# Kernel optimization log

Measured on AMD Instinct MI355X. Metric: run time of the kernel, lower is better.

## Reference

```python
import jax, jax.numpy as jnp
import numpy as np

N = 100000   # nodes
E = 600000   # edges per graph
F = 512      # node_features == input_size
H = 256      # n_hidden
H2 = 128     # n_hidden // 2
O = 1        # output_size
EPS = 1e-5


def gcn_conv(x, W, b, src, dst, n):
    # PyG GCNConv: add self-loops, symmetric normalization, then scatter-add.
    xw = x @ W                                   # [N, out]
    loop = jnp.arange(n)
    s = jnp.concatenate([src, loop])
    d = jnp.concatenate([dst, loop])
    deg = jax.ops.segment_sum(jnp.ones_like(d, jnp.float32), d, num_segments=n)
    dis = jnp.where(deg > 0, jax.lax.rsqrt(jnp.maximum(deg, 1.0)), 0.0)
    norm = dis[s] * dis[d]                       # [E+N]
    msg = xw[s] * norm[:, None]
    return jax.ops.segment_sum(msg, d, num_segments=n) + b


def sage_conv(x, Wl, bl, Wr, src, dst, n):
    # PyG SAGEConv (mean aggr): lin_l(mean_neigh) + lin_r(x); lin_r has no bias.
    agg = jax.ops.segment_sum(x[src], dst, num_segments=n)
    cnt = jax.ops.segment_sum(jnp.ones_like(dst, jnp.float32), dst, num_segments=n)
    mean = agg / jnp.maximum(cnt, 1.0)[:, None]
    return mean @ Wl + bl + x @ Wr


def layer_norm(x, w, b):
    mu = jnp.mean(x, axis=-1, keepdims=True)
    var = jnp.mean(jnp.square(x - mu), axis=-1, keepdims=True)
    return (x - mu) * jax.lax.rsqrt(var + EPS) * w + b


def mlp(x, Wm1, bm1, ln_w, ln_b, Wm2, bm2):
    h = layer_norm(x @ Wm1 + bm1, ln_w, ln_b)
    return h @ Wm2 + bm2


def setup_inputs() -> dict:
    key = jax.random.key(0)
    ks = jax.random.split(key, 22)
    s = 0.05
    d = {}
    d["x"] = jax.random.normal(ks[0], (N, F), jnp.float32)
    d["x1"] = jax.random.normal(ks[1], (N, F), jnp.float32)
    d["edge_index"] = jax.random.randint(ks[2], (2, E), 0, N)
    d["edge_index1"] = jax.random.randint(ks[3], (2, E), 0, N)
    # conv1_1 / conv2_1: GCNConv(F -> H)
    d["Wg1"] = jax.random.normal(ks[4], (F, H), jnp.float32) * s
    d["bg1"] = jnp.zeros((H,), jnp.float32)
    d["Wg2"] = jax.random.normal(ks[5], (F, H), jnp.float32) * s
    d["bg2"] = jnp.zeros((H,), jnp.float32)
    # conv1_2 / conv2_2: SAGEConv(H -> H2)
    d["Wl1"] = jax.random.normal(ks[6], (H, H2), jnp.float32) * s
    d["bl1"] = jnp.zeros((H2,), jnp.float32)
    d["Wr1"] = jax.random.normal(ks[7], (H, H2), jnp.float32) * s
    d["Wl2"] = jax.random.normal(ks[8], (H, H2), jnp.float32) * s
    d["bl2"] = jnp.zeros((H2,), jnp.float32)
    d["Wr2"] = jax.random.normal(ks[9], (H, H2), jnp.float32) * s
    # shared MLP: Linear(H2,H2) -> LayerNorm(H2) -> Linear(H2,O)
    d["Wm1"] = jax.random.normal(ks[10], (H2, H2), jnp.float32) * s
    d["bm1"] = jnp.zeros((H2,), jnp.float32)
    d["ln_w"] = jnp.ones((H2,), jnp.float32)
    d["ln_b"] = jnp.zeros((H2,), jnp.float32)
    d["Wm2"] = jax.random.normal(ks[11], (H2, O), jnp.float32) * s
    d["bm2"] = jnp.zeros((O,), jnp.float32)
    return d


def reference(x, x1, edge_index, edge_index1, Wg1, bg1, Wg2, bg2,
              Wl1, bl1, Wr1, Wl2, bl2, Wr2, Wm1, bm1, ln_w, ln_b, Wm2, bm2):
    src, dst = edge_index[0], edge_index[1]
    src1, dst1 = edge_index1[0], edge_index1[1]
    n = x.shape[0]

    h = gcn_conv(x, Wg1, bg1, src, dst, n)
    h0 = jax.nn.relu(h)                          # x0 = relu(conv1_1)
    g = gcn_conv(x1, Wg2, bg2, src1, dst1, n)
    g0 = jax.nn.relu(g)                          # x1_0 = relu(conv2_1)

    x0 = h0 + g0
    a = jax.nn.relu(sage_conv(x0, Wl1, bl1, Wr1, src, dst, n))
    a = mlp(a, Wm1, bm1, ln_w, ln_b, Wm2, bm2)   # [N, 1]
    a = jnp.squeeze(a)                            # [N]

    g1 = g0 + g                                   # x1_0 + x1 (pre-relu conv2_1)
    b_ = jax.nn.relu(sage_conv(g1, Wl2, bl2, Wr2, src1, dst1, n))
    b_ = mlp(b_, Wm1, bm1, ln_w, ln_b, Wm2, bm2)
    b_ = jnp.squeeze(b_)                          # [N]

    cat = jnp.concatenate([a, b_], axis=0)        # [2N]
    out = jnp.mean(cat)
    return out[None, None]                        # [1, 1]
```

## Files before the change

kernel.cpp:

```cpp
#include <hip/hip_runtime.h>

#define NN 100000
#define EE 600000
#define FF 512
#define HH 256
#define HD2 128

typedef unsigned short u16;
typedef unsigned int u32;
typedef __attribute__((ext_vector_type(4))) float f32x4;
typedef __attribute__((ext_vector_type(8))) short bf16x8;

__device__ __forceinline__ float bflo(u32 u){ return __uint_as_float(u << 16); }
__device__ __forceinline__ float bfhi(u32 u){ return __uint_as_float(u & 0xffff0000u); }
__device__ __forceinline__ u32 f2bf(float x){
  u32 u = __float_as_uint(x);
  return (u + 0x7FFFu + ((u >> 16) & 1u)) >> 16;
}
__device__ __forceinline__ u32 pack2(float x, float y){ return f2bf(x) | (f2bf(y) << 16); }

__global__ void zero_int_k(int* __restrict__ p, int n){
  int i = blockIdx.x * 256 + threadIdx.x;
  int st = gridDim.x * 256;
  for (; i < n; i += st) p[i] = 0;
}

__global__ void count_deg_k(const int* __restrict__ dst, int* __restrict__ deg, int nE){
  int e = blockIdx.x * 256 + threadIdx.x;
  if (e < nE) atomicAdd(&deg[dst[e]], 1);
}

__global__ __launch_bounds__(256) void scan1_k(const int* __restrict__ deg, int* __restrict__ out,
                                               int* __restrict__ aux, int n){
  __shared__ int sm[256];
  const int t = threadIdx.x;
  const int base = blockIdx.x * 1024 + t * 4;
  int v0 = (base+0) < n ? deg[base+0] : 0;
  int v1 = (base+1) < n ? deg[base+1] : 0;
  int v2 = (base+2) < n ? deg[base+2] : 0;
  int v3 = (base+3) < n ? deg[base+3] : 0;
  int s = v0 + v1 + v2 + v3;
  sm[t] = s;
  __syncthreads();
  for (int off = 1; off < 256; off <<= 1){
    int x = (t >= off) ? sm[t - off] : 0;
    __syncthreads();
    sm[t] += x;
    __syncthreads();
  }
  if (t == 255) aux[blockIdx.x] = sm[255];
  int run = sm[t] - s;
  if (base+0 < n) out[base+0] = run;            run += v0;
  if (base+1 < n) out[base+1] = run;            run += v1;
  if (base+2 < n) out[base+2] = run;            run += v2;
  if (base+3 < n) out[base+3] = run;
}
__global__ void scan2_k(int* __restrict__ aux, int nchunks){
  if (threadIdx.x == 0){
    int run = 0;
    for (int i = 0; i < nchunks; ++i){ int t = aux[i]; aux[i] = run; run += t; }
  }
}
__global__ void scan3_k(int* __restrict__ out, const int* __restrict__ aux, int n){
  int i = blockIdx.x * 256 + threadIdx.x;
  if (i < n) out[i] += aux[i >> 10];
}

__global__ void csr_fill_k(const int* __restrict__ src, const int* __restrict__ dst,
                           const int* __restrict__ rp, int* __restrict__ fill,
                           int* __restrict__ csr, int nE){
  int e = blockIdx.x * 256 + threadIdx.x;
  if (e >= nE) return;
  int d = dst[e];
  int pos = rp[d] + atomicAdd(&fill[d], 1);
  csr[pos] = src[e];
}

__global__ void wtcvt_k(const float* __restrict__ W, u16* __restrict__ WT,
                        int K, int nmask, int nshift, int total){
  int idx = blockIdx.x * 256 + threadIdx.x;
  if (idx >= total) return;
  int k = idx >> nshift, n = idx & nmask;
  WT[(size_t)n * K + k] = (u16)f2bf(W[idx]);
}

__global__ __launch_bounds__(256) void gemm_xw_k(
    const float* __restrict__ A, const u16* __restrict__ BT,
    u16* __restrict__ C, int M)
{
  __shared__ u16 As[128][40];
  __shared__ u16 Bs[128][40];
  const int tid = threadIdx.x;
  const int w = tid >> 6, lane = tid & 63;
  const int row0 = blockIdx.x * 128, col0 = blockIdx.y * 128;
  const int wr = (w >> 1) * 64, wc = (w & 1) * 64;
  const int sar = tid >> 1, sak = (tid & 1) * 16;
  const int lrow = lane & 15, lk = (lane >> 4) * 8;
  f32x4 acc[4][4];
#pragma unroll
  for (int i = 0; i < 4; ++i)
#pragma unroll
    for (int j = 0; j < 4; ++j)
#pragma unroll
      for (int q = 0; q < 4; ++q) acc[i][j][q] = 0.f;

  const bool aval = (row0 + sar) < M;
  const float* apb = A + (size_t)(row0 + sar) * FF + sak;

  for (int kb = 0; kb < FF; kb += 32){
    if (aval){
      const float4* ap = (const float4*)(apb + kb);
      float4 v0 = ap[0], v1 = ap[1], v2 = ap[2], v3 = ap[3];
      uint4 p0 = make_uint4(pack2(v0.x,v0.y), pack2(v0.z,v0.w), pack2(v1.x,v1.y), pack2(v1.z,v1.w));
      uint4 p1 = make_uint4(pack2(v2.x,v2.y), pack2(v2.z,v2.w), pack2(v3.x,v3.y), pack2(v3.z,v3.w));
      *(uint4*)&As[sar][sak]     = p0;
      *(uint4*)&As[sar][sak + 8] = p1;
    } else {
      uint4 z = make_uint4(0,0,0,0);
      *(uint4*)&As[sar][sak]     = z;
      *(uint4*)&As[sar][sak + 8] = z;
    }
    for (int c = tid; c < 512; c += 256){
      int n = c >> 2, part = c & 3;
      uint4 bv = *(const uint4*)(BT + (size_t)(col0 + n) * FF + kb + part * 8);
      *(uint4*)&Bs[n][part * 8] = bv;
    }
    __syncthreads();
    bf16x8 af[4], bfr[4];
#pragma unroll
    for (int mt = 0; mt < 4; ++mt) af[mt]  = *(const bf16x8*)&As[wr + mt*16 + lrow][lk];
#pragma unroll
    for (int nt = 0; nt < 4; ++nt) bfr[nt] = *(const bf16x8*)&Bs[wc + nt*16 + lrow][lk];
#pragma unroll
    for (int mt = 0; mt < 4; ++mt)
#pragma unroll
      for (int nt = 0; nt < 4; ++nt)
        acc[mt][nt] = __builtin_amdgcn_mfma_f32_16x16x32_bf16(af[mt], bfr[nt], acc[mt][nt], 0, 0, 0);
    __syncthreads();
  }
  const int orow = (lane >> 4) * 4, ocol = lane & 15;
#pragma unroll
  for (int mt = 0; mt < 4; ++mt)
#pragma unroll
    for (int i = 0; i < 4; ++i){
      int r = row0 + wr + mt*16 + orow + i;
      if (r < M){
        u16* cp = C + (size_t)r * HH + col0 + wc + ocol;
#pragma unroll
        for (int nt = 0; nt < 4; ++nt)
          cp[nt * 16] = (u16)f2bf(acc[mt][nt][i]);
      }
    }
}

__global__ __launch_bounds__(256) void gcn_agg_k(
    const u16* __restrict__ XW, const int* __restrict__ rp,
    const int* __restrict__ deg, const int* __restrict__ csr,
    const float* __restrict__ bias, u16* __restrict__ H, int n)
{
  const int d = blockIdx.x * 4 + (threadIdx.x >> 6);
  if (d >= n) return;
  const int lane = threadIdx.x & 63;
  const int dg = deg[d];
  const float disd = rsqrtf((float)dg + 1.0f);
  const uint2* xw2 = (const uint2*)XW;
  uint2 sv = xw2[(size_t)d * 64 + lane];
  const float sw = disd * disd;
  float a0 = bflo(sv.x) * sw, a1 = bfhi(sv.x) * sw;
  float a2 = bflo(sv.y) * sw, a3 = bfhi(sv.y) * sw;
  const int s0 = rp[d], s1 = s0 + dg;
  for (int i = s0; i < s1; ++i){
    int s = csr[i];
    float wgt = rsqrtf((float)deg[s] + 1.0f) * disd;
    uint2 v = xw2[(size_t)s * 64 + lane];
    a0 = fmaf(bflo(v.x), wgt, a0); a1 = fmaf(bfhi(v.x), wgt, a1);
    a2 = fmaf(bflo(v.y), wgt, a2); a3 = fmaf(bfhi(v.y), wgt, a3);
  }
  const float4 bv = *(const float4*)(bias + lane * 4);
  a0 += bv.x; a1 += bv.y; a2 += bv.z; a3 += bv.w;
  uint2 o; o.x = pack2(a0, a1); o.y = pack2(a2, a3);
  ((uint2*)H)[(size_t)d * 64 + lane] = o;
}

__global__ __launch_bounds__(256) void sage_mean_k(
    const u16* __restrict__ X, const int* __restrict__ rp,
    const int* __restrict__ deg, const int* __restrict__ csr,
    u16* __restrict__ Mo, int n)
{
  const int d = blockIdx.x * 4 + (threadIdx.x >> 6);
  if (d >= n) return;
  const int lane = threadIdx.x & 63;
  const int dg = deg[d];
  const uint2* x2 = (const uint2*)X;
  float a0 = 0.f, a1 = 0.f, a2 = 0.f, a3 = 0.f;
  const int s0 = rp[d], s1 = s0 + dg;
  for (int i = s0; i < s1; ++i){
    int s = csr[i];
    uint2 v = x2[(size_t)s * 64 + lane];
    a0 += bflo(v.x); a1 += bfhi(v.x);
    a2 += bflo(v.y); a3 += bfhi(v.y);
  }
  const float sc = 1.0f / (float)(dg > 0 ? dg : 1);
  uint2 o; o.x = pack2(a0 * sc, a1 * sc); o.y = pack2(a2 * sc, a3 * sc);
  ((uint2*)Mo)[(size_t)d * 64 + lane] = o;
}

__global__ void combine_k(u32* __restrict__ X0, u32* __restrict__ G1,
                          const u32* __restrict__ H1, const u32* __restrict__ H2)
{
  int i = blockIdx.x * 256 + threadIdx.x;
  u32 uh = H1[i], ug = H2[i];
  float h0 = bflo(uh), h1 = bfhi(uh), g0 = bflo(ug), g1 = bfhi(ug);
  float rh0 = fmaxf(h0, 0.f), rh1 = fmaxf(h1, 0.f);
  float rg0 = fmaxf(g0, 0.f), rg1 = fmaxf(g1, 0.f);
  X0[i] = pack2(rh0 + rg0, rh1 + rg1);
  G1[i] = pack2(rg0 + g0, rg1 + g1);
}

__global__ __launch_bounds__(256) void sage_gemm_k(
    const u16* __restrict__ A1, const u16* __restrict__ A2,
    const u16* __restrict__ B1T, const u16* __restrict__ B2T,
    const float* __restrict__ bias, u16* __restrict__ S, int M)
{
  __shared__ u16 As[128][40];
  __shared__ u16 Bs[128][40];
  const int tid = threadIdx.x;
  const int w = tid >> 6, lane = tid & 63;
  const int row0 = blockIdx.x * 128;
  const int wr = (w >> 1) * 64, wc = (w & 1) * 64;
  const int lrow = lane & 15, lk = (lane >> 4) * 8;
  f32x4 acc[4][4];
#pragma unroll
  for (int i = 0; i < 4; ++i)
#pragma unroll
    for (int j = 0; j < 4; ++j)
#pragma unroll
      for (int q = 0; q < 4; ++q) acc[i][j][q] = 0.f;

  for (int pass = 0; pass < 2; ++pass){
    const u16* Ap = pass ? A2 : A1;
    const u16* Bp = pass ? B2T : B1T;
    for (int kb = 0; kb < HH; kb += 32){
      for (int c = tid; c < 512; c += 256){
        int r = c >> 2, part = c & 3;
        int grow = row0 + r;
        uint4 v = make_uint4(0,0,0,0);
        if (grow < M) v = *(const uint4*)(Ap + (size_t)grow * HH + kb + part * 8);
        *(uint4*)&As[r][part * 8] = v;
      }
      for (int c = tid; c < 512; c += 256){
        int n = c >> 2, part = c & 3;
        uint4 v = *(const uint4*)(Bp + (size_t)n * HH + kb + part * 8);
        *(uint4*)&Bs[n][part * 8] = v;
      }
      __syncthreads();
      bf16x8 af[4], bfr[4];
#pragma unroll
      for (int mt = 0; mt < 4; ++mt) af[mt]  = *(const bf16x8*)&As[wr + mt*16 + lrow][lk];
#pragma unroll
      for (int nt = 0; nt < 4; ++nt) bfr[nt] = *(const bf16x8*)&Bs[wc + nt*16 + lrow][lk];
#pragma unroll
      for (int mt = 0; mt < 4; ++mt)
#pragma unroll
        for (int nt = 0; nt < 4; ++nt)
          acc[mt][nt] = __builtin_amdgcn_mfma_f32_16x16x32_bf16(af[mt], bfr[nt], acc[mt][nt], 0, 0, 0);
      __syncthreads();
    }
  }
  const int orow = (lane >> 4) * 4, ocol = lane & 15;
#pragma unroll
  for (int mt = 0; mt < 4; ++mt)
#pragma unroll
    for (int i = 0; i < 4; ++i){
      int r = row0 + wr + mt*16 + orow + i;
      if (r < M){
        u16* cp = S + (size_t)r * HD2 + wc + ocol;
#pragma unroll
        for (int nt = 0; nt < 4; ++nt){
          float v = acc[mt][nt][i] + bias[wc + nt*16 + ocol];
          cp[nt * 16] = (u16)f2bf(fmaxf(v, 0.f));
        }
      }
    }
}

__global__ __launch_bounds__(256) void mlp_reduce_k(
    const u16* __restrict__ Xin,
    const float* __restrict__ Wm1, const float* __restrict__ bm1,
    const float* __restrict__ lnw, const float* __restrict__ lnb,
    const float* __restrict__ Wm2, const float* __restrict__ bm2,
    double* __restrict__ partial, int M)
{
  __shared__ u32 Wsh[HD2 * HD2 / 2];
  __shared__ float Bsh[HD2];
  __shared__ float LWs[HD2];
  __shared__ float LBs[HD2];
  __shared__ float W2s[HD2];
  __shared__ float arow[4][HD2];
  __shared__ double wsum[4];
  const int tid = threadIdx.x;
  const float2* Wsrc = (const float2*)Wm1;
  for (int i = tid; i < HD2 * HD2 / 2; i += 256){
    float2 w = Wsrc[i];
    Wsh[i] = pack2(w.x, w.y);
  }
  if (tid < HD2){
    Bsh[tid] = bm1[tid];
    LWs[tid] = lnw[tid];
    LBs[tid] = lnb[tid];
    W2s[tid] = Wm2[tid];
  }
  __syncthreads();
  const int lane = tid & 63, wv = tid >> 6;
  const int j0 = lane << 1;
  const float bm2v = bm2[0];
  const u32* xin = (const u32*)Xin;
  double local = 0.0;
  for (int base = blockIdx.x * 4; base < M; base += gridDim.x * 4){
    const int node = base + wv;
    const bool active = node < M;
    if (active){
      u32 u = xin[(size_t)node * 64 + lane];
      arow[wv][j0] = bflo(u);
      arow[wv][j0 + 1] = bfhi(u);
    }
    __syncthreads();
    if (active){
      float2 tb = *(const float2*)&Bsh[j0];
      float t0 = tb.x, t1 = tb.y;
#pragma unroll 8
      for (int k = 0; k < HD2; ++k){
        float ak = arow[wv][k];
        u32 w = Wsh[k * 64 + lane];
        t0 = fmaf(ak, bflo(w), t0);
        t1 = fmaf(ak, bfhi(w), t1);
      }
      float s = t0 + t1;
#pragma unroll
      for (int off = 32; off > 0; off >>= 1) s += __shfl_xor(s, off);
      float mu = s * (1.0f / HD2);
      float v0 = t0 - mu, v1 = t1 - mu;
      float vs = v0 * v0 + v1 * v1;
#pragma unroll
      for (int off = 32; off > 0; off >>= 1) vs += __shfl_xor(vs, off);
      float rs = rsqrtf(vs * (1.0f / HD2) + 1e-5f);
      float2 lw = *(const float2*)&LWs[j0];
      float2 lb = *(const float2*)&LBs[j0];
      float2 w2 = *(const float2*)&W2s[j0];
      float y0 = fmaf(v0 * rs, lw.x, lb.x);
      float y1 = fmaf(v1 * rs, lw.y, lb.y);
      float p = y0 * w2.x + y1 * w2.y;
#pragma unroll
      for (int off = 32; off > 0; off >>= 1) p += __shfl_xor(p, off);
      if (lane == 0) local += (double)(p + bm2v);
    }
    __syncthreads();
  }
  if (lane == 0) wsum[wv] = local;
  __syncthreads();
  if (tid == 0)
    partial[blockIdx.x] = wsum[0] + wsum[1] + wsum[2] + wsum[3];
}

__global__ __launch_bounds__(256) void final_reduce_k(
    const double* __restrict__ P, u32* __restrict__ out)
{
  __shared__ double sm[256];
  const int tid = threadIdx.x;
  double s = P[tid] + P[tid + 256] + P[tid + 512] + P[tid + 768];
  sm[tid] = s;
  __syncthreads();
  for (int h = 128; h > 0; h >>= 1){
    if (tid < h) sm[tid] += sm[tid + h];
    __syncthreads();
  }
  if (tid == 0){
    float v = (float)(sm[0] * (1.0 / (2.0 * (double)NN)));
    u32 bf = f2bf(v);
    out[0] = (bf << 16) | bf;
  }
}

extern "C" void kernel_launch(void* const* d_in, const int* in_sizes, int n_in,
                              void* d_out, int out_size, void* d_ws, size_t ws_size,
                              hipStream_t stream)
{
  const float* x   = (const float*)d_in[0];
  const float* x1  = (const float*)d_in[1];
  const int* ei  = (const int*)d_in[2];
  const int* ei1 = (const int*)d_in[3];
  const float* Wg1 = (const float*)d_in[4];
  const float* bg1 = (const float*)d_in[5];
  const float* Wg2 = (const float*)d_in[6];
  const float* bg2 = (const float*)d_in[7];
  const float* Wl1 = (const float*)d_in[8];
  const float* bl1 = (const float*)d_in[9];
  const float* Wr1 = (const float*)d_in[10];
  const float* Wl2 = (const float*)d_in[11];
  const float* bl2 = (const float*)d_in[12];
  const float* Wr2 = (const float*)d_in[13];
  const float* Wm1 = (const float*)d_in[14];
  const float* bm1 = (const float*)d_in[15];
  const float* lnw = (const float*)d_in[16];
  const float* lnb = (const float*)d_in[17];
  const float* Wm2 = (const float*)d_in[18];
  const float* bm2 = (const float*)d_in[19];

  const int* src1 = ei,  * dst1 = ei + EE;
  const int* src2 = ei1, * dst2 = ei1 + EE;

  u16* U0 = (u16*)d_ws;
  u16* U1 = U0 + (size_t)NN * HH;
  u16* U2 = U1 + (size_t)NN * HH;
  u16* U3 = U2 + (size_t)NN * HH;
  u16* U4 = U3 + (size_t)NN * HH;
  u16* U5 = U4 + (size_t)NN * HD2;
  u16* WG1T = U5 + (size_t)NN * HD2;
  u16* WG2T = WG1T + HH * FF;
  u16* WL1T = WG2T + HH * FF;
  u16* WR1T = WL1T + HD2 * HH;
  u16* WL2T = WR1T + HD2 * HH;
  u16* WR2T = WL2T + HD2 * HH;
  int* deg1 = (int*)(WR2T + HD2 * HH);
  int* deg2 = deg1 + NN;
  int* fill1 = deg2 + NN;
  int* fill2 = fill1 + NN;
  int* rp1 = fill2 + NN;
  int* rp2 = rp1 + NN;
  int* aux1 = rp2 + NN;
  int* aux2 = aux1 + 128;
  int* csr1 = aux2 + 128;
  int* csr2 = csr1 + EE;
  double* P = (double*)(csr2 + EE);

  const int eblk = (EE + 255) / 256;
  const int nchunks = (NN + 1023) / 1024;

  zero_int_k<<<512, 256, 0, stream>>>(deg1, 4 * NN);
  count_deg_k<<<eblk, 256, 0, stream>>>(dst1, deg1, EE);
  count_deg_k<<<eblk, 256, 0, stream>>>(dst2, deg2, EE);
  scan1_k<<<nchunks, 256, 0, stream>>>(deg1, rp1, aux1, NN);
  scan1_k<<<nchunks, 256, 0, stream>>>(deg2, rp2, aux2, NN);
  scan2_k<<<1, 64, 0, stream>>>(aux1, nchunks);
  scan2_k<<<1, 64, 0, stream>>>(aux2, nchunks);
  scan3_k<<<(NN + 255) / 256, 256, 0, stream>>>(rp1, aux1, NN);
  scan3_k<<<(NN + 255) / 256, 256, 0, stream>>>(rp2, aux2, NN);
  csr_fill_k<<<eblk, 256, 0, stream>>>(src1, dst1, rp1, fill1, csr1, EE);
  csr_fill_k<<<eblk, 256, 0, stream>>>(src2, dst2, rp2, fill2, csr2, EE);

  wtcvt_k<<<512, 256, 0, stream>>>(Wg1, WG1T, FF, HH - 1, 8, FF * HH);
  wtcvt_k<<<512, 256, 0, stream>>>(Wg2, WG2T, FF, HH - 1, 8, FF * HH);
  wtcvt_k<<<128, 256, 0, stream>>>(Wl1, WL1T, HH, HD2 - 1, 7, HH * HD2);
  wtcvt_k<<<128, 256, 0, stream>>>(Wr1, WR1T, HH, HD2 - 1, 7, HH * HD2);
  wtcvt_k<<<128, 256, 0, stream>>>(Wl2, WL2T, HH, HD2 - 1, 7, HH * HD2);
  wtcvt_k<<<128, 256, 0, stream>>>(Wr2, WR2T, HH, HD2 - 1, 7, HH * HD2);

  dim3 ggrid((NN + 127) / 128, HH / 128);
  gemm_xw_k<<<ggrid, 256, 0, stream>>>(x,  WG1T, U0, NN);
  gemm_xw_k<<<ggrid, 256, 0, stream>>>(x1, WG2T, U1, NN);

  gcn_agg_k<<<NN / 4, 256, 0, stream>>>(U0, rp1, deg1, csr1, bg1, U2, NN);
  gcn_agg_k<<<NN / 4, 256, 0, stream>>>(U1, rp2, deg2, csr2, bg2, U3, NN);

  combine_k<<<NN * HH / 512, 256, 0, stream>>>((u32*)U0, (u32*)U1, (const u32*)U2, (const u32*)U3);

  sage_mean_k<<<NN / 4, 256, 0, stream>>>(U0, rp1, deg1, csr1, U2, NN);
  sage_mean_k<<<NN / 4, 256, 0, stream>>>(U1, rp2, deg2, csr2, U3, NN);

  sage_gemm_k<<<(NN + 127) / 128, 256, 0, stream>>>(U2, U0, WL1T, WR1T, bl1, U4, NN);
  sage_gemm_k<<<(NN + 127) / 128, 256, 0, stream>>>(U3, U1, WL2T, WR2T, bl2, U5, NN);

  mlp_reduce_k<<<512, 256, 0, stream>>>(U4, Wm1, bm1, lnw, lnb, Wm2, bm2, P, NN);
  mlp_reduce_k<<<512, 256, 0, stream>>>(U5, Wm1, bm1, lnw, lnb, Wm2, bm2, P + 512, NN);

  final_reduce_k<<<1, 256, 0, stream>>>(P, (u32*)d_out);
}
```

Before: 1.531 ms.

## Compute MLP head with bf16 MFMA and fold LayerNorm into final projection

Replaces the scalar per-node MLP kernel with an MFMA-based kernel. Each wave computes 16 nodes at a time against a transposed bf16 Wm1 held in padded shared memory. The LayerNorm affine and the final 128->1 projection are folded algebraically into precomputed constants, so only sums, variance and one dot product are needed per node. Both graph branches are processed in one launch over the contiguous U4/U5 buffers, with U0 reused as scratch for the transposed weight. This trades a small change in rounding order for far fewer LDS reads and scalar FMAs.

```diff
diff --git a/kernel.cpp b/kernel.cpp
--- a/kernel.cpp
+++ b/kernel.cpp
@@ -284,82 +284,95 @@
     }
 }
 
-__global__ __launch_bounds__(256) void mlp_reduce_k(
+__global__ __launch_bounds__(256) void mlp_mfma_k(
     const u16* __restrict__ Xin,
-    const float* __restrict__ Wm1, const float* __restrict__ bm1,
+    const u16* __restrict__ W1T,
+    const float* __restrict__ bm1,
     const float* __restrict__ lnw, const float* __restrict__ lnb,
     const float* __restrict__ Wm2, const float* __restrict__ bm2,
     double* __restrict__ partial, int M)
 {
-  __shared__ u32 Wsh[HD2 * HD2 / 2];
-  __shared__ float Bsh[HD2];
-  __shared__ float LWs[HD2];
-  __shared__ float LBs[HD2];
-  __shared__ float W2s[HD2];
-  __shared__ float arow[4][HD2];
+  __shared__ u16 Wsh[HD2][136];
   __shared__ double wsum[4];
   const int tid = threadIdx.x;
-  const float2* Wsrc = (const float2*)Wm1;
-  for (int i = tid; i < HD2 * HD2 / 2; i += 256){
-    float2 w = Wsrc[i];
-    Wsh[i] = pack2(w.x, w.y);
-  }
-  if (tid < HD2){
-    Bsh[tid] = bm1[tid];
-    LWs[tid] = lnw[tid];
-    LBs[tid] = lnb[tid];
-    W2s[tid] = Wm2[tid];
-  }
+  const int lane = tid & 63, wv = tid >> 6;
+  const int g = lane >> 4, cn = lane & 15;
+
+  for (int i = tid; i < HD2 * 16; i += 256){
+    int j = i >> 4, c = i & 15;
+    *(uint4*)&Wsh[j][c * 8] = ((const uint4*)W1T)[i];
+  }
+
+  f32x4 b1v[8], c1v[8];
+  float S1 = 0.f, C0 = 0.f;
+#pragma unroll
+  for (int jt = 0; jt < 8; ++jt){
+    int j = jt * 16 + g * 4;
+    float4 bb = *(const float4*)&bm1[j];
+    float4 lw = *(const float4*)&lnw[j];
+    float4 lb = *(const float4*)&lnb[j];
+    float4 w2 = *(const float4*)&Wm2[j];
+    b1v[jt][0] = bb.x; b1v[jt][1] = bb.y; b1v[jt][2] = bb.z; b1v[jt][3] = bb.w;
+    c1v[jt][0] = lw.x * w2.x; c1v[jt][1] = lw.y * w2.y;
+    c1v[jt][2] = lw.z * w2.z; c1v[jt][3] = lw.w * w2.w;
+    S1 += c1v[jt][0] + c1v[jt][1] + c1v[jt][2] + c1v[jt][3];
+    C0 += lb.x * w2.x + lb.y * w2.y + lb.z * w2.z + lb.w * w2.w;
+  }
+  S1 += __shfl_xor(S1, 16); S1 += __shfl_xor(S1, 32);
+  C0 += __shfl_xor(C0, 16); C0 += __shfl_xor(C0, 32);
+  const float bm2v = bm2[0];
   __syncthreads();
-  const int lane = tid & 63, wv = tid >> 6;
-  const int j0 = lane << 1;
-  const float bm2v = bm2[0];
-  const u32* xin = (const u32*)Xin;
+
   double local = 0.0;
-  for (int base = blockIdx.x * 4; base < M; base += gridDim.x * 4){
-    const int node = base + wv;
-    const bool active = node < M;
-    if (active){
-      u32 u = xin[(size_t)node * 64 + lane];
-      arow[wv][j0] = bflo(u);
-      arow[wv][j0 + 1] = bfhi(u);
-    }
-    __syncthreads();
-    if (active){
-      float2 tb = *(const float2*)&Bsh[j0];
-      float t0 = tb.x, t1 = tb.y;
-#pragma unroll 8
-      for (int k = 0; k < HD2; ++k){
-        float ak = arow[wv][k];
-        u32 w = Wsh[k * 64 + lane];
-        t0 = fmaf(ak, bflo(w), t0);
-        t1 = fmaf(ak, bfhi(w), t1);
-      }
-      float s = t0 + t1;
-#pragma unroll
-      for (int off = 32; off > 0; off >>= 1) s += __shfl_xor(s, off);
-      float mu = s * (1.0f / HD2);
-      float v0 = t0 - mu, v1 = t1 - mu;
-      float vs = v0 * v0 + v1 * v1;
-#pragma unroll
-      for (int off = 32; off > 0; off >>= 1) vs += __shfl_xor(vs, off);
-      float rs = rsqrtf(vs * (1.0f / HD2) + 1e-5f);
-      float2 lw = *(const float2*)&LWs[j0];
-      float2 lb = *(const float2*)&LBs[j0];
-      float2 w2 = *(const float2*)&W2s[j0];
-      float y0 = fmaf(v0 * rs, lw.x, lb.x);
-      float y1 = fmaf(v1 * rs, lw.y, lb.y);
-      float p = y0 * w2.x + y1 * w2.y;
-#pragma unroll
-      for (int off = 32; off > 0; off >>= 1) p += __shfl_xor(p, off);
-      if (lane == 0) local += (double)(p + bm2v);
-    }
-    __syncthreads();
-  }
+  const int stride = gridDim.x * 64;
+  for (int base = blockIdx.x * 64 + wv * 16; base < M; base += stride){
+    const int node = base + cn;
+    const bool nv = node < M;
+    f32x4 acc[8];
+#pragma unroll
+    for (int jt = 0; jt < 8; ++jt){ acc[jt][0]=0.f; acc[jt][1]=0.f; acc[jt][2]=0.f; acc[jt][3]=0.f; }
+#pragma unroll
+    for (int ks = 0; ks < 4; ++ks){
+      bf16x8 bfv = {0,0,0,0,0,0,0,0};
+      if (nv) bfv = *(const bf16x8*)(Xin + (size_t)node * HD2 + ks * 32 + g * 8);
+#pragma unroll
+      for (int jt = 0; jt < 8; ++jt){
+        bf16x8 afr = *(const bf16x8*)&Wsh[jt * 16 + cn][ks * 32 + g * 8];
+        acc[jt] = __builtin_amdgcn_mfma_f32_16x16x32_bf16(afr, bfv, acc[jt], 0, 0, 0);
+      }
+    }
+    float s = 0.f;
+#pragma unroll
+    for (int jt = 0; jt < 8; ++jt){
+#pragma unroll
+      for (int r = 0; r < 4; ++r){
+        acc[jt][r] += b1v[jt][r];
+        s += acc[jt][r];
+      }
+    }
+    s += __shfl_xor(s, 16); s += __shfl_xor(s, 32);
+    const float mu = s * (1.0f / HD2);
+    float vs = 0.f, d1 = 0.f;
+#pragma unroll
+    for (int jt = 0; jt < 8; ++jt){
+#pragma unroll
+      for (int r = 0; r < 4; ++r){
+        float dv = acc[jt][r] - mu;
+        vs = fmaf(dv, dv, vs);
+        d1 = fmaf(acc[jt][r], c1v[jt][r], d1);
+      }
+    }
+    vs += __shfl_xor(vs, 16); vs += __shfl_xor(vs, 32);
+    d1 += __shfl_xor(d1, 16); d1 += __shfl_xor(d1, 32);
+    const float rs = rsqrtf(vs * (1.0f / HD2) + 1e-5f);
+    const float p = rs * (d1 - mu * S1) + C0 + bm2v;
+    if (nv && g == 0) local += (double)p;
+  }
+#pragma unroll
+  for (int off = 32; off > 0; off >>= 1) local += __shfl_xor(local, off);
   if (lane == 0) wsum[wv] = local;
   __syncthreads();
-  if (tid == 0)
-    partial[blockIdx.x] = wsum[0] + wsum[1] + wsum[2] + wsum[3];
+  if (tid == 0) partial[blockIdx.x] = wsum[0] + wsum[1] + wsum[2] + wsum[3];
 }
 
 __global__ __launch_bounds__(256) void final_reduce_k(
@@ -432,6 +445,7 @@
   int* csr1 = aux2 + 128;
   int* csr2 = csr1 + EE;
   double* P = (double*)(csr2 + EE);
+  u16* WM1T = U0;
 
   const int eblk = (EE + 255) / 256;
   const int nchunks = (NN + 1023) / 1024;
@@ -470,8 +484,9 @@
   sage_gemm_k<<<(NN + 127) / 128, 256, 0, stream>>>(U2, U0, WL1T, WR1T, bl1, U4, NN);
   sage_gemm_k<<<(NN + 127) / 128, 256, 0, stream>>>(U3, U1, WL2T, WR2T, bl2, U5, NN);
 
-  mlp_reduce_k<<<512, 256, 0, stream>>>(U4, Wm1, bm1, lnw, lnb, Wm2, bm2, P, NN);
-  mlp_reduce_k<<<512, 256, 0, stream>>>(U5, Wm1, bm1, lnw, lnb, Wm2, bm2, P + 512, NN);
+  wtcvt_k<<<64, 256, 0, stream>>>(Wm1, WM1T, HD2, HD2 - 1, 7, HD2 * HD2);
+
+  mlp_mfma_k<<<1024, 256, 0, stream>>>(U4, WM1T, bm1, lnw, lnb, Wm2, bm2, P, 2 * NN);
 
   final_reduce_k<<<1, 256, 0, stream>>>(P, (u32*)d_out);
 }
```

Result: faster. 1.265 ms (-17.4%).
